# Optimization experiments

Hardware: AMD Instinct MI355X
Metric: run time of the kernel (lower is better)

Reference implementation:

```python
import jax, jax.numpy as jnp
import numpy as np

N_NODES = 50000
D = 128
L = 3  # layers
R = 4  # relations
E = 200000  # edges per relation
LN_EPS = 1e-5
NEG_SLOPE = 0.2


def setup_inputs() -> dict:
    key = jax.random.key(0)
    ks = jax.random.split(key, 12)
    s = 1.0 / np.sqrt(D)  # xavier-ish scale
    return {
        "h": jax.random.normal(ks[0], (N_NODES, D), jnp.float32),
        "edge_src": jax.random.randint(ks[1], (R, E), 0, N_NODES, jnp.int32),
        "edge_dst": jax.random.randint(ks[2], (R, E), 0, N_NODES, jnp.int32),
        "W_src": jax.random.normal(ks[3], (L, R, D, D), jnp.float32) * s,
        "W_dst": jax.random.normal(ks[4], (L, R, D, D), jnp.float32) * s,
        "attn_l": jax.random.normal(ks[5], (L, R, D), jnp.float32) * s,
        "attn_r": jax.random.normal(ks[6], (L, R, D), jnp.float32) * s,
        "gat_bias": jax.random.normal(ks[7], (L, R, D), jnp.float32) * 0.02,
        "ntype_bias": jax.random.normal(ks[8], (L, D), jnp.float32) * 0.02,
        "ln_gamma": jnp.ones((L, D), jnp.float32),
        "ln_beta": jnp.zeros((L, D), jnp.float32),
    }


def _gat_rel(x, Wsrc, Wdst, al, ar, b, src, dst):
    # single-head DGL GATConv with bipartite (src, dst) feats (same node set here)
    n = x.shape[0]
    hs = x @ Wsrc  # [N, D] projected source feats
    hd = x @ Wdst  # [N, D] projected dest feats
    el = (hs * al).sum(-1)  # [N]
    er = (hd * ar).sum(-1)  # [N]
    e = jax.nn.leaky_relu(el[src] + er[dst], NEG_SLOPE)  # [E]
    # edge softmax over incoming edges of each dst node
    m = jax.lax.stop_gradient(jax.ops.segment_max(e, dst, num_segments=n))
    a = jnp.exp(e - m[dst])
    denom = jax.ops.segment_sum(a, dst, num_segments=n)
    w = a / denom[dst]  # [E] attention weights
    out = jax.ops.segment_sum(hs[src] * w[:, None], dst, num_segments=n)  # [N, D]
    return out + b


def _layer_norm(x, g, b):
    mu = x.mean(-1, keepdims=True)
    var = ((x - mu) ** 2).mean(-1, keepdims=True)
    return (x - mu) * jax.lax.rsqrt(var + LN_EPS) * g + b


def reference(h, edge_src, edge_dst, W_src, W_dst, attn_l, attn_r,
              gat_bias, ntype_bias, ln_gamma, ln_beta):
    x = h
    n_layers = W_src.shape[0]
    gat_vmapped = jax.vmap(_gat_rel, in_axes=(None, 0, 0, 0, 0, 0, 0, 0))
    for l in range(n_layers):
        rel_out = gat_vmapped(x, W_src[l], W_dst[l], attn_l[l], attn_r[l],
                              gat_bias[l], edge_src, edge_dst)  # [R, N, D]
        hsum = rel_out.sum(0) + ntype_bias[l]  # HeteroGraphConv 'sum' + ntype bias
        if l < n_layers - 1:
            hsum = jax.nn.relu(hsum)  # activation on all but final layer
        # mean over heads (num_heads=1) is identity; then per-layer LayerNorm
        x = _layer_norm(hsum, ln_gamma[l], ln_beta[l])
    return x
```

## Files before the change

kernel.cpp:

```cpp
#include <hip/hip_runtime.h>

#define NN 50000
#define DIM 128
#define NREL 4
#define NEDGE 200000
#define NLAYER 3
#define SNB 196

typedef short s16x8 __attribute__((ext_vector_type(8)));
typedef float f32x4 __attribute__((ext_vector_type(4)));

__device__ __forceinline__ unsigned short f2bf(float f) {
    union { float f; unsigned u; } c; c.f = f;
    unsigned u = c.u + 0x7fffu + ((c.u >> 16) & 1u);
    return (unsigned short)(u >> 16);
}
__device__ __forceinline__ float lo_bf(unsigned u) {
    union { float f; unsigned u; } c; c.u = u << 16; return c.f;
}
__device__ __forceinline__ float hi_bf(unsigned u) {
    union { float f; unsigned u; } c; c.u = u & 0xffff0000u; return c.f;
}

__global__ __launch_bounds__(256) void k_constf(float* __restrict__ out, int n, float v) {
    int i = blockIdx.x * 256 + threadIdx.x;
    if (i < n) out[i] = v;
}

__global__ __launch_bounds__(256) void k_count(const int* __restrict__ dst, int* __restrict__ counts) {
    int r = blockIdx.y;
    int i = blockIdx.x * 256 + threadIdx.x;
    if (i < NEDGE) {
        int d = dst[r * NEDGE + i];
        if ((unsigned)d < NN) atomicAdd(&counts[r * NN + d], 1);
    }
}

__global__ __launch_bounds__(256) void k_s1(const int* __restrict__ counts, int* __restrict__ bsum) {
    int r = blockIdx.y, b = blockIdx.x;
    int i = b * 256 + threadIdx.x;
    int v = (i < NN) ? counts[r * NN + i] : 0;
    #pragma unroll
    for (int m = 1; m < 64; m <<= 1) v += __shfl_xor(v, m);
    __shared__ int ws[4];
    int wid = threadIdx.x >> 6, lane = threadIdx.x & 63;
    if (lane == 0) ws[wid] = v;
    __syncthreads();
    if (threadIdx.x == 0) bsum[r * SNB + b] = ws[0] + ws[1] + ws[2] + ws[3];
}

__global__ __launch_bounds__(256) void k_s2(const int* __restrict__ bsum, int* __restrict__ boff) {
    int r = threadIdx.x >> 6;
    int lane = threadIdx.x & 63;
    int carry = 0;
    for (int c0 = 0; c0 < SNB; c0 += 64) {
        int b = c0 + lane;
        int v = (b < SNB) ? bsum[r * SNB + b] : 0;
        int inc = v;
        #pragma unroll
        for (int d = 1; d < 64; d <<= 1) {
            int t = __shfl_up(inc, d);
            if (lane >= d) inc += t;
        }
        if (b < SNB) boff[r * SNB + b] = carry + inc - v;
        carry += __shfl(inc, 63);
    }
}

__global__ __launch_bounds__(256) void k_s3(const int* __restrict__ counts, const int* __restrict__ boff,
                                            int* __restrict__ row_ptr, int* __restrict__ nxt) {
    int r = blockIdx.y, b = blockIdx.x;
    int i = b * 256 + threadIdx.x;
    int v = (i < NN) ? counts[r * NN + i] : 0;
    int lane = threadIdx.x & 63, wid = threadIdx.x >> 6;
    int inc = v;
    #pragma unroll
    for (int d = 1; d < 64; d <<= 1) {
        int t = __shfl_up(inc, d);
        if (lane >= d) inc += t;
    }
    __shared__ int ws[4];
    if (lane == 63) ws[wid] = inc;
    __syncthreads();
    int woff = 0;
    #pragma unroll
    for (int w = 0; w < 4; ++w) woff += (w < wid) ? ws[w] : 0;
    if (i < NN) {
        int ex = boff[r * SNB + b] + woff + inc - v;
        row_ptr[r * (NN + 1) + i] = ex;
        nxt[r * NN + i] = ex;
    }
    if (b == 0 && threadIdx.x == 0) row_ptr[r * (NN + 1) + NN] = NEDGE;
}

__global__ __launch_bounds__(256) void k_fill(const int* __restrict__ src, const int* __restrict__ dst,
                                              int* __restrict__ nxt, int* __restrict__ csr) {
    int r = blockIdx.y;
    int i = blockIdx.x * 256 + threadIdx.x;
    if (i < NEDGE) {
        int d = dst[r * NEDGE + i];
        if ((unsigned)d >= NN) return;
        int pos = atomicAdd(&nxt[r * NN + d], 1);
        if ((unsigned)pos < NEDGE) csr[r * NEDGE + pos] = src[r * NEDGE + i];
    }
}

__global__ __launch_bounds__(256) void k_prep(const float* __restrict__ Wsrc,
                                              const float* __restrict__ Wdst,
                                              const float* __restrict__ al,
                                              const float* __restrict__ ar,
                                              const float* __restrict__ ntb,
                                              const float* __restrict__ gb,
                                              const float* __restrict__ x,
                                              unsigned short* __restrict__ wf,
                                              float* __restrict__ wl,
                                              float* __restrict__ wr,
                                              float* __restrict__ biasc,
                                              unsigned short* __restrict__ xb) {
    int b = blockIdx.x;
    const int PL = NLAYER * 512;
    if (b < PL) {
        int l = b / 512;
        int t = b % 512;
        if (t < 256) {
            int idx = t * 256 + threadIdx.x;
            int jj = idx & 7, lane = (idx >> 3) & 63, s = (idx >> 9) & 3, tt = (idx >> 11) & 7, r = idx >> 14;
            int k = s * 32 + ((lane >> 4) << 3) + jj;
            int n = tt * 16 + (lane & 15);
            wf[l * 65536 + idx] = f2bf(Wsrc[((size_t)(l * NREL + r) * DIM + k) * DIM + n]);
        } else if (t < 384) {
            int gw = (t - 256) * 4 + (threadIdx.x >> 6);
            int lane = threadIdx.x & 63;
            int r = gw >> 7, k = gw & 127;
            const float* wrow = Wsrc + (((size_t)(l * NREL + r) * DIM + k) * DIM);
            const float* arow = al + (l * NREL + r) * DIM;
            float s = wrow[lane * 2] * arow[lane * 2] + wrow[lane * 2 + 1] * arow[lane * 2 + 1];
            #pragma unroll
            for (int m = 1; m < 64; m <<= 1) s += __shfl_xor(s, m);
            if (lane == 0) wl[l * 512 + gw] = s;
        } else {
            int gw = (t - 384) * 4 + (threadIdx.x >> 6);
            int lane = threadIdx.x & 63;
            int r = gw >> 7, k = gw & 127;
            const float* wrow = Wdst + (((size_t)(l * NREL + r) * DIM + k) * DIM);
            const float* arow = ar + (l * NREL + r) * DIM;
            float s = wrow[lane * 2] * arow[lane * 2] + wrow[lane * 2 + 1] * arow[lane * 2 + 1];
            #pragma unroll
            for (int m = 1; m < 64; m <<= 1) s += __shfl_xor(s, m);
            if (lane == 0) wr[l * 512 + gw] = s;
        }
    } else if (b < PL + 2) {
        int t = (b - PL) * 256 + threadIdx.x;
        if (t < NLAYER * DIM) {
            int l = t >> 7, k = t & 127;
            float s = ntb[t];
            #pragma unroll
            for (int r = 0; r < NREL; ++r) s += gb[(l * NREL + r) * DIM + k];
            biasc[t] = s;
        }
    } else {
        int i = ((b - PL - 2) * 256 + threadIdx.x) * 4;
        f32x4 v = *(const f32x4*)(x + i);
        unsigned short o[4];
        #pragma unroll
        for (int j = 0; j < 4; ++j) o[j] = f2bf(v[j]);
        *(ushort2*)(xb + i) = make_ushort2(o[0], o[1]);
        *(ushort2*)(xb + i + 2) = make_ushort2(o[2], o[3]);
    }
}

__global__ __launch_bounds__(256) void k_er0(const float* __restrict__ x,
                                             const float* __restrict__ wl,
                                             const float* __restrict__ wr,
                                             float* __restrict__ el,
                                             float* __restrict__ er) {
    int oct = threadIdx.x >> 3, ol = threadIdx.x & 7;
    int n = blockIdx.x * 32 + oct;
    if (n >= NN) return;
    int f0 = ol * 16;
    const float* xp = x + (size_t)n * DIM + f0;
    f32x4 xv[4];
    #pragma unroll
    for (int k = 0; k < 4; ++k) xv[k] = *(const f32x4*)(xp + 4 * k);
    #pragma unroll
    for (int r = 0; r < NREL; ++r) {
        float sl = 0.f, sr = 0.f;
        #pragma unroll
        for (int k = 0; k < 4; ++k) {
            f32x4 lv = *(const f32x4*)(wl + r * DIM + f0 + 4 * k);
            f32x4 rv = *(const f32x4*)(wr + r * DIM + f0 + 4 * k);
            sl += xv[k][0] * lv[0] + xv[k][1] * lv[1] + xv[k][2] * lv[2] + xv[k][3] * lv[3];
            sr += xv[k][0] * rv[0] + xv[k][1] * rv[1] + xv[k][2] * rv[2] + xv[k][3] * rv[3];
        }
        sl += __shfl_xor(sl, 1); sl += __shfl_xor(sl, 2); sl += __shfl_xor(sl, 4);
        sr += __shfl_xor(sr, 1); sr += __shfl_xor(sr, 2); sr += __shfl_xor(sr, 4);
        if (ol == 0) { el[r * NN + n] = sl; er[r * NN + n] = sr; }
    }
}

__global__ __launch_bounds__(512) void k_fused(const unsigned short* __restrict__ xb,
                                               const float* __restrict__ el,
                                               const float* __restrict__ er,
                                               const int* __restrict__ row_ptr,
                                               const int* __restrict__ csr,
                                               const unsigned short* __restrict__ wf,
                                               const float* __restrict__ biasc,
                                               const float* __restrict__ lng,
                                               const float* __restrict__ lnb,
                                               const float* __restrict__ wl,
                                               const float* __restrict__ wr,
                                               float* __restrict__ dout,
                                               unsigned short* __restrict__ xb2,
                                               float* __restrict__ el2,
                                               float* __restrict__ er2,
                                               int l, int last) {
    __shared__ s16x8 lds_a[16 * 64];
    int tid = threadIdx.x;

    {
        int pair = tid >> 3;
        int ol   = tid & 7;
        int g    = ol >> 2;
        int fl   = ol & 3;
        int nd   = pair >> 2;
        int r    = pair & 3;
        int n    = blockIdx.x * 16 + nd;
        int f0   = fl * 32;

        int start = row_ptr[r * (NN + 1) + n];
        int end   = row_ptr[r * (NN + 1) + n + 1];
        if (start < 0) start = 0;
        if (end > NEDGE) end = NEDGE;
        int deg = end - start;

        float ern = er[r * NN + n];
        const int* cp = csr + r * NEDGE;
        const float* elp = el + r * NN;

        f32x4 av[8] = {{0,0,0,0},{0,0,0,0},{0,0,0,0},{0,0,0,0},
                       {0,0,0,0},{0,0,0,0},{0,0,0,0},{0,0,0,0}};
        float denom = 0.f;
        int e = start + g;
        if (e < end) {
            int s0 = cp[e]; if ((unsigned)s0 >= NN) s0 = 0;
            float e0v = elp[s0];
            const uint4* hp = (const uint4*)(xb + (size_t)s0 * DIM + f0);
            uint4 xa = hp[0], xbv = hp[1], xc = hp[2], xd = hp[3];
            for (; e < end; e += 2) {
                int i1 = e + 2; i1 = (i1 < end) ? i1 : start;
                int s1 = cp[i1]; if ((unsigned)s1 >= NN) s1 = 0;
                float e1v = elp[s1];
                const uint4* hp1 = (const uint4*)(xb + (size_t)s1 * DIM + f0);
                uint4 ya = hp1[0], yb = hp1[1], yc = hp1[2], yd = hp1[3];

                float ev = e0v + ern;
                ev = ev >= 0.f ? ev : 0.2f * ev;
                ev = fminf(fmaxf(ev, -60.f), 60.f);
                float p = __expf(ev);
                denom += p;
                av[0][0] += p * lo_bf(xa.x); av[0][1] += p * hi_bf(xa.x);
                av[0][2] += p * lo_bf(xa.y); av[0][3] += p * hi_bf(xa.y);
                av[1][0] += p * lo_bf(xa.z); av[1][1] += p * hi_bf(xa.z);
                av[1][2] += p * lo_bf(xa.w); av[1][3] += p * hi_bf(xa.w);
                av[2][0] += p * lo_bf(xbv.x); av[2][1] += p * hi_bf(xbv.x);
                av[2][2] += p * lo_bf(xbv.y); av[2][3] += p * hi_bf(xbv.y);
                av[3][0] += p * lo_bf(xbv.z); av[3][1] += p * hi_bf(xbv.z);
                av[3][2] += p * lo_bf(xbv.w); av[3][3] += p * hi_bf(xbv.w);
                av[4][0] += p * lo_bf(xc.x); av[4][1] += p * hi_bf(xc.x);
                av[4][2] += p * lo_bf(xc.y); av[4][3] += p * hi_bf(xc.y);
                av[5][0] += p * lo_bf(xc.z); av[5][1] += p * hi_bf(xc.z);
                av[5][2] += p * lo_bf(xc.w); av[5][3] += p * hi_bf(xc.w);
                av[6][0] += p * lo_bf(xd.x); av[6][1] += p * hi_bf(xd.x);
                av[6][2] += p * lo_bf(xd.y); av[6][3] += p * hi_bf(xd.y);
                av[7][0] += p * lo_bf(xd.z); av[7][1] += p * hi_bf(xd.z);
                av[7][2] += p * lo_bf(xd.w); av[7][3] += p * hi_bf(xd.w);
                e0v = e1v; xa = ya; xbv = yb; xc = yc; xd = yd;
            }
        }
        denom += __shfl_xor(denom, 4);
        #pragma unroll
        for (int q = 0; q < 8; ++q) {
            #pragma unroll
            for (int j = 0; j < 4; ++j) av[q][j] += __shfl_xor(av[q][j], 4);
        }
        float inv = (deg > 0) ? (1.0f / denom) : 0.f;
        if (g == 0) {
            #pragma unroll
            for (int q = 0; q < 4; ++q) {
                s16x8 o;
                #pragma unroll
                for (int j = 0; j < 4; ++j) {
                    o[j]     = (short)f2bf(av[2 * q][j] * inv);
                    o[j + 4] = (short)f2bf(av[2 * q + 1][j] * inv);
                }
                lds_a[(r * 4 + fl) * 64 + q * 16 + nd] = o;
            }
        }
    }
    __syncthreads();

    int wv = tid >> 6, lane = tid & 63;
    int quad = lane >> 4, n16 = lane & 15;
    f32x4 acc = {0.f, 0.f, 0.f, 0.f};
    {
        const s16x8* wfp = (const s16x8*)wf + (size_t)l * NREL * 2048;
        #pragma unroll
        for (int sp = 0; sp < 16; ++sp) {
            s16x8 a = lds_a[sp * 64 + lane];
            const s16x8* wb = wfp + (size_t)(sp >> 2) * 2048;
            int sl = sp & 3;
            s16x8 b = wb[(wv * 4 + sl) * 64 + lane];
            acc = __builtin_amdgcn_mfma_f32_16x16x32_bf16(a, b, acc, 0, 0, 0);
        }
    }
    __syncthreads();
    float* Cl = (float*)lds_a;
    {
        #pragma unroll
        for (int reg = 0; reg < 4; ++reg) {
            int row = quad * 4 + reg;
            Cl[row * DIM + wv * 16 + n16] = acc[reg];
        }
    }
    __syncthreads();

    {
        int nd2 = tid >> 5;
        int sub = tid & 31;
        int f   = sub * 4;
        int n2  = blockIdx.x * 16 + nd2;

        float t[4];
        #pragma unroll
        for (int j = 0; j < 4; ++j) t[j] = Cl[nd2 * DIM + f + j] + biasc[l * DIM + f + j];
        if (!last) {
            #pragma unroll
            for (int j = 0; j < 4; ++j) t[j] = fmaxf(t[j], 0.f);
        }
        float s1 = 0.f;
        #pragma unroll
        for (int j = 0; j < 4; ++j) s1 += t[j];
        s1 += __shfl_xor(s1, 1); s1 += __shfl_xor(s1, 2);
        s1 += __shfl_xor(s1, 4); s1 += __shfl_xor(s1, 8);
        s1 += __shfl_xor(s1, 16);
        float mean = s1 * (1.0f / 128.0f);
        float s2 = 0.f;
        #pragma unroll
        for (int j = 0; j < 4; ++j) { t[j] -= mean; s2 += t[j] * t[j]; }
        s2 += __shfl_xor(s2, 1); s2 += __shfl_xor(s2, 2);
        s2 += __shfl_xor(s2, 4); s2 += __shfl_xor(s2, 8);
        s2 += __shfl_xor(s2, 16);
        float rs = rsqrtf(s2 * (1.0f / 128.0f) + 1e-5f);

        float y[4];
        #pragma unroll
        for (int j = 0; j < 4; ++j)
            y[j] = t[j] * rs * lng[l * DIM + f + j] + lnb[l * DIM + f + j];

        if (last) {
            float* op = dout + (size_t)n2 * DIM + f;
            f32x4 v0;
            v0[0] = y[0]; v0[1] = y[1]; v0[2] = y[2]; v0[3] = y[3];
            *(f32x4*)op = v0;
        } else {
            unsigned pk0 = (unsigned)f2bf(y[0]) | ((unsigned)f2bf(y[1]) << 16);
            unsigned pk1 = (unsigned)f2bf(y[2]) | ((unsigned)f2bf(y[3]) << 16);
            uint2 v; v.x = pk0; v.y = pk1;
            *(uint2*)(xb2 + (size_t)n2 * DIM + f) = v;

            const float* wlp = wl + (l + 1) * 512;
            const float* wrp = wr + (l + 1) * 512;
            #pragma unroll
            for (int rp = 0; rp < NREL; ++rp) {
                float sl_ = 0.f, sr_ = 0.f;
                #pragma unroll
                for (int j = 0; j < 4; ++j) {
                    sl_ += y[j] * wlp[rp * DIM + f + j];
                    sr_ += y[j] * wrp[rp * DIM + f + j];
                }
                sl_ += __shfl_xor(sl_, 1); sl_ += __shfl_xor(sl_, 2);
                sl_ += __shfl_xor(sl_, 4); sl_ += __shfl_xor(sl_, 8);
                sl_ += __shfl_xor(sl_, 16);
                sr_ += __shfl_xor(sr_, 1); sr_ += __shfl_xor(sr_, 2);
                sr_ += __shfl_xor(sr_, 4); sr_ += __shfl_xor(sr_, 8);
                sr_ += __shfl_xor(sr_, 16);
                if (sub == 0) {
                    el2[rp * NN + n2] = sl_;
                    er2[rp * NN + n2] = sr_;
                }
            }
        }
    }
}

extern "C" void kernel_launch(void* const* d_in, const int* in_sizes, int n_in,
                              void* d_out, int out_size, void* d_ws, size_t ws_size,
                              hipStream_t stream) {
    const float* h        = (const float*)d_in[0];
    const int*   edge_src = (const int*)d_in[1];
    const int*   edge_dst = (const int*)d_in[2];
    const float* W_src    = (const float*)d_in[3];
    const float* W_dst    = (const float*)d_in[4];
    const float* attn_l   = (const float*)d_in[5];
    const float* attn_r   = (const float*)d_in[6];
    const float* gat_bias = (const float*)d_in[7];
    const float* ntype_b  = (const float*)d_in[8];
    const float* ln_g     = (const float*)d_in[9];
    const float* ln_b     = (const float*)d_in[10];

    if (n_in < 11) return;
    if (in_sizes[0] != NN * DIM) return;
    if (in_sizes[1] != NREL * NEDGE || in_sizes[2] != NREL * NEDGE) return;
    if (in_sizes[3] != NLAYER * NREL * DIM * DIM || in_sizes[4] != NLAYER * NREL * DIM * DIM) return;
    if (in_sizes[5] != NLAYER * NREL * DIM || in_sizes[6] != NLAYER * NREL * DIM) return;
    if (in_sizes[7] != NLAYER * NREL * DIM || in_sizes[8] != NLAYER * DIM) return;
    if (out_size != NN * DIM) return;

    auto align256 = [](size_t x) { return (x + 255) & ~(size_t)255; };
    size_t szElEr = align256((size_t)NREL * NN * 4);
    size_t szXbf  = align256((size_t)NN * DIM * 2);
    size_t szWlr  = align256((size_t)NLAYER * 512 * 4);
    size_t szBc   = align256((size_t)NLAYER * DIM * 4);
    size_t szWf   = align256((size_t)NLAYER * NREL * DIM * DIM * 2);
    size_t szRp   = align256((size_t)NREL * (NN + 1) * 4);
    size_t szNxt  = align256((size_t)NREL * NN * 4);
    size_t szCsr  = align256((size_t)NREL * NEDGE * 4);
    size_t szScn  = align256((size_t)NREL * SNB * 4) * 2;
    size_t need = 4 * szElEr + 2 * szXbf + 2 * szWlr + szBc + szWf + szRp + szNxt + szCsr + szScn;

    if (ws_size < need) {
        k_constf<<<(NN * DIM + 255) / 256, 256, 0, stream>>>((float*)d_out, NN * DIM, 100.0f);
        return;
    }

    char* base = (char*)d_ws;
    size_t off = 0;
    auto alloc = [&](size_t bytes) -> char* { char* p = base + off; off += align256(bytes); return p; };

    float* el   = (float*)alloc((size_t)NREL * NN * 4);
    float* er   = (float*)alloc((size_t)NREL * NN * 4);
    float* el2  = (float*)alloc((size_t)NREL * NN * 4);
    float* er2  = (float*)alloc((size_t)NREL * NN * 4);
    unsigned short* xbf  = (unsigned short*)alloc((size_t)NN * DIM * 2);
    unsigned short* xbf2 = (unsigned short*)alloc((size_t)NN * DIM * 2);
    float* wl    = (float*)alloc((size_t)NLAYER * 512 * 4);
    float* wr    = (float*)alloc((size_t)NLAYER * 512 * 4);
    float* biasc = (float*)alloc((size_t)NLAYER * DIM * 4);
    unsigned short* wfrag = (unsigned short*)alloc((size_t)NLAYER * NREL * DIM * DIM * 2);
    int* rowp = (int*)alloc((size_t)NREL * (NN + 1) * 4);
    int* nxt  = (int*)alloc((size_t)NREL * NN * 4);
    int* csr  = (int*)alloc((size_t)NREL * NEDGE * 4);
    int* bsum = (int*)alloc((size_t)NREL * SNB * 4);
    int* boff = (int*)alloc((size_t)NREL * SNB * 4);

    (void)hipMemsetAsync(nxt, 0, (size_t)NREL * NN * 4, stream);
    k_count<<<dim3((NEDGE + 255) / 256, NREL), 256, 0, stream>>>(edge_dst, nxt);
    k_s1<<<dim3(SNB, NREL), 256, 0, stream>>>(nxt, bsum);
    k_s2<<<1, 256, 0, stream>>>(bsum, boff);
    k_s3<<<dim3(SNB, NREL), 256, 0, stream>>>(nxt, boff, rowp, nxt);
    k_fill<<<dim3((NEDGE + 255) / 256, NREL), 256, 0, stream>>>(edge_src, edge_dst, nxt, csr);
    k_prep<<<NLAYER * 512 + 2 + NN * DIM / 1024, 256, 0, stream>>>(
        W_src, W_dst, attn_l, attn_r, ntype_b, gat_bias, h, wfrag, wl, wr, biasc, xbf);
    k_er0<<<(NN + 31) / 32, 256, 0, stream>>>(h, wl, wr, el, er);

    float* dout = (float*)d_out;
    k_fused<<<NN / 16, 512, 0, stream>>>(xbf, el, er, rowp, csr, wfrag, biasc, ln_g, ln_b,
                                         wl, wr, dout, xbf2, el2, er2, 0, 0);
    k_fused<<<NN / 16, 512, 0, stream>>>(xbf2, el2, er2, rowp, csr, wfrag, biasc, ln_g, ln_b,
                                         wl, wr, dout, xbf, el, er, 1, 0);
    k_fused<<<NN / 16, 512, 0, stream>>>(xbf, el, er, rowp, csr, wfrag, biasc, ln_g, ln_b,
                                         wl, wr, dout, xbf2, el2, er2, 2, 1);
}
```

Before: 400.7 us.

## Halve fused-kernel block to 8 nodes with 256 threads and two MFMA tiles per wave

Shrinks each fused block from 16 nodes/512 threads to 8 nodes/256 threads, doubling the grid, and sets launch bounds to allow 8 blocks per CU. Each of the 4 waves now computes two 16-column MFMA output tiles. The unused 8 rows of the 16-row MFMA A operand are zero-filled. The aim is finer-grained scheduling and better latency hiding for the irregular gather phase. The cost is that half of every MFMA is wasted on padding rows, and weight fragments are reloaded twice as often across blocks.

Result: slower. 526.5 us (+31.4%).

```diff
diff --git a/kernel.cpp b/kernel.cpp
--- a/kernel.cpp
+++ b/kernel.cpp
@@ -6,6 +6,7 @@
 #define NEDGE 200000
 #define NLAYER 3
 #define SNB 196
+#define NODES_PER_BLK 8
 
 typedef short s16x8 __attribute__((ext_vector_type(8)));
 typedef float f32x4 __attribute__((ext_vector_type(4)));
@@ -198,7 +199,7 @@
     }
 }
 
-__global__ __launch_bounds__(512) void k_fused(const unsigned short* __restrict__ xb,
+__global__ __launch_bounds__(256, 8) void k_fused(const unsigned short* __restrict__ xb,
                                                const float* __restrict__ el,
                                                const float* __restrict__ er,
                                                const int* __restrict__ row_ptr,
@@ -224,7 +225,7 @@
         int fl   = ol & 3;
         int nd   = pair >> 2;
         int r    = pair & 3;
-        int n    = blockIdx.x * 16 + nd;
+        int n    = blockIdx.x * NODES_PER_BLK + nd;
         int f0   = fl * 32;
 
         int start = row_ptr[r * (NN + 1) + n];
@@ -295,31 +296,43 @@
                 }
                 lds_a[(r * 4 + fl) * 64 + q * 16 + nd] = o;
             }
+        } else {
+            s16x8 z = {0, 0, 0, 0, 0, 0, 0, 0};
+            #pragma unroll
+            for (int q = 0; q < 4; ++q)
+                lds_a[(r * 4 + fl) * 64 + q * 16 + nd + 8] = z;
         }
     }
     __syncthreads();
 
     int wv = tid >> 6, lane = tid & 63;
     int quad = lane >> 4, n16 = lane & 15;
-    f32x4 acc = {0.f, 0.f, 0.f, 0.f};
+    f32x4 acc0 = {0.f, 0.f, 0.f, 0.f}, acc1 = {0.f, 0.f, 0.f, 0.f};
     {
         const s16x8* wfp = (const s16x8*)wf + (size_t)l * NREL * 2048;
+        int t0c = wv * 2, t1c = wv * 2 + 1;
         #pragma unroll
         for (int sp = 0; sp < 16; ++sp) {
             s16x8 a = lds_a[sp * 64 + lane];
             const s16x8* wb = wfp + (size_t)(sp >> 2) * 2048;
             int sl = sp & 3;
-            s16x8 b = wb[(wv * 4 + sl) * 64 + lane];
-            acc = __builtin_amdgcn_mfma_f32_16x16x32_bf16(a, b, acc, 0, 0, 0);
+            s16x8 b0 = wb[(t0c * 4 + sl) * 64 + lane];
+            s16x8 b1 = wb[(t1c * 4 + sl) * 64 + lane];
+            acc0 = __builtin_amdgcn_mfma_f32_16x16x32_bf16(a, b0, acc0, 0, 0, 0);
+            acc1 = __builtin_amdgcn_mfma_f32_16x16x32_bf16(a, b1, acc1, 0, 0, 0);
         }
     }
     __syncthreads();
     float* Cl = (float*)lds_a;
     {
+        int t0c = wv * 2, t1c = wv * 2 + 1;
         #pragma unroll
         for (int reg = 0; reg < 4; ++reg) {
             int row = quad * 4 + reg;
-            Cl[row * DIM + wv * 16 + n16] = acc[reg];
+            if (row < NODES_PER_BLK) {
+                Cl[row * DIM + t0c * 16 + n16] = acc0[reg];
+                Cl[row * DIM + t1c * 16 + n16] = acc1[reg];
+            }
         }
     }
     __syncthreads();
@@ -328,7 +341,7 @@
         int nd2 = tid >> 5;
         int sub = tid & 31;
         int f   = sub * 4;
-        int n2  = blockIdx.x * 16 + nd2;
+        int n2  = blockIdx.x * NODES_PER_BLK + nd2;
 
         float t[4];
         #pragma unroll
@@ -464,10 +477,10 @@
     k_er0<<<(NN + 31) / 32, 256, 0, stream>>>(h, wl, wr, el, er);
 
     float* dout = (float*)d_out;
-    k_fused<<<NN / 16, 512, 0, stream>>>(xbf, el, er, rowp, csr, wfrag, biasc, ln_g, ln_b,
+    k_fused<<<NN / NODES_PER_BLK, 256, 0, stream>>>(xbf, el, er, rowp, csr, wfrag, biasc, ln_g, ln_b,
                                          wl, wr, dout, xbf2, el2, er2, 0, 0);
-    k_fused<<<NN / 16, 512, 0, stream>>>(xbf2, el2, er2, rowp, csr, wfrag, biasc, ln_g, ln_b,
+    k_fused<<<NN / NODES_PER_BLK, 256, 0, stream>>>(xbf2, el2, er2, rowp, csr, wfrag, biasc, ln_g, ln_b,
                                          wl, wr, dout, xbf, el, er, 1, 0);
-    k_fused<<<NN / 16, 512, 0, stream>>>(xbf, el, er, rowp, csr, wfrag, biasc, ln_g, ln_b,
+    k_fused<<<NN / NODES_PER_BLK, 256, 0, stream>>>(xbf, el, er, rowp, csr, wfrag, biasc, ln_g, ln_b,
                                          wl, wr, dout, xbf2, el2, er2, 2, 1);
 }
```

## Process 32 nodes per 256-thread block with 2x2 MFMA tiles per wave

Applied to the files above, without the earlier changes.

The fused layer kernel now handles 32 destination nodes per block with 256 threads instead of 16 nodes with 512 threads. The edge-gather phase drops the two-way edge split and its shuffle reduction, so each thread walks all edges of its (node, relation, feature-slice) serially over two passes. In the GEMM phase each wave computes a 2x2 block of 16x16 MFMA tiles, so every weight fragment loaded is reused across twice as many rows. The cost is less parallelism in the gather, a longer serial edge loop per thread, more registers per thread, and half as many threads in flight to hide gather latency.

Result: faster. 367.6 us (-8.3%).

```diff
diff --git a/kernel.cpp b/kernel.cpp
--- a/kernel.cpp
+++ b/kernel.cpp
@@ -6,6 +6,7 @@
 #define NEDGE 200000
 #define NLAYER 3
 #define SNB 196
+#define NODES_PER_BLK 32
 
 typedef short s16x8 __attribute__((ext_vector_type(8)));
 typedef float f32x4 __attribute__((ext_vector_type(4)));
@@ -198,7 +199,7 @@
     }
 }
 
-__global__ __launch_bounds__(512) void k_fused(const unsigned short* __restrict__ xb,
+__global__ __launch_bounds__(256) void k_fused(const unsigned short* __restrict__ xb,
                                                const float* __restrict__ el,
                                                const float* __restrict__ er,
                                                const int* __restrict__ row_ptr,
@@ -214,121 +215,124 @@
                                                float* __restrict__ el2,
                                                float* __restrict__ er2,
                                                int l, int last) {
-    __shared__ s16x8 lds_a[16 * 64];
+    __shared__ s16x8 lds_a[2 * 16 * 64];
     int tid = threadIdx.x;
 
-    {
-        int pair = tid >> 3;
-        int ol   = tid & 7;
-        int g    = ol >> 2;
-        int fl   = ol & 3;
+    for (int p = 0; p < 2; ++p) {
+        int pair = tid >> 2;
+        int ol   = tid & 3;
         int nd   = pair >> 2;
         int r    = pair & 3;
-        int n    = blockIdx.x * 16 + nd;
-        int f0   = fl * 32;
-
-        int start = row_ptr[r * (NN + 1) + n];
-        int end   = row_ptr[r * (NN + 1) + n + 1];
+        int n    = blockIdx.x * NODES_PER_BLK + p * 16 + nd;
+        int f0   = ol * 32;
+
+        int valid = (n < NN);
+        int nc = valid ? n : 0;
+        int start = row_ptr[r * (NN + 1) + nc];
+        int end   = valid ? row_ptr[r * (NN + 1) + nc + 1] : start;
         if (start < 0) start = 0;
         if (end > NEDGE) end = NEDGE;
         int deg = end - start;
 
-        float ern = er[r * NN + n];
+        float ern = er[r * NN + nc];
         const int* cp = csr + r * NEDGE;
         const float* elp = el + r * NN;
 
         f32x4 av[8] = {{0,0,0,0},{0,0,0,0},{0,0,0,0},{0,0,0,0},
                        {0,0,0,0},{0,0,0,0},{0,0,0,0},{0,0,0,0}};
         float denom = 0.f;
-        int e = start + g;
-        if (e < end) {
-            int s0 = cp[e]; if ((unsigned)s0 >= NN) s0 = 0;
-            float e0v = elp[s0];
+        if (deg > 0) {
+            int s0 = cp[start]; if ((unsigned)s0 >= NN) s0 = 0;
+            float e0 = elp[s0];
             const uint4* hp = (const uint4*)(xb + (size_t)s0 * DIM + f0);
             uint4 xa = hp[0], xbv = hp[1], xc = hp[2], xd = hp[3];
-            for (; e < end; e += 2) {
-                int i1 = e + 2; i1 = (i1 < end) ? i1 : start;
+            for (int e = 0; e < deg; ++e) {
+                int i1 = start + e + 1; i1 = (i1 < end) ? i1 : start;
                 int s1 = cp[i1]; if ((unsigned)s1 >= NN) s1 = 0;
-                float e1v = elp[s1];
+                float e1 = elp[s1];
                 const uint4* hp1 = (const uint4*)(xb + (size_t)s1 * DIM + f0);
                 uint4 ya = hp1[0], yb = hp1[1], yc = hp1[2], yd = hp1[3];
 
-                float ev = e0v + ern;
+                float ev = e0 + ern;
                 ev = ev >= 0.f ? ev : 0.2f * ev;
                 ev = fminf(fmaxf(ev, -60.f), 60.f);
-                float p = __expf(ev);
-                denom += p;
-                av[0][0] += p * lo_bf(xa.x); av[0][1] += p * hi_bf(xa.x);
-                av[0][2] += p * lo_bf(xa.y); av[0][3] += p * hi_bf(xa.y);
-                av[1][0] += p * lo_bf(xa.z); av[1][1] += p * hi_bf(xa.z);
-                av[1][2] += p * lo_bf(xa.w); av[1][3] += p * hi_bf(xa.w);
-                av[2][0] += p * lo_bf(xbv.x); av[2][1] += p * hi_bf(xbv.x);
-                av[2][2] += p * lo_bf(xbv.y); av[2][3] += p * hi_bf(xbv.y);
-                av[3][0] += p * lo_bf(xbv.z); av[3][1] += p * hi_bf(xbv.z);
-                av[3][2] += p * lo_bf(xbv.w); av[3][3] += p * hi_bf(xbv.w);
-                av[4][0] += p * lo_bf(xc.x); av[4][1] += p * hi_bf(xc.x);
-                av[4][2] += p * lo_bf(xc.y); av[4][3] += p * hi_bf(xc.y);
-                av[5][0] += p * lo_bf(xc.z); av[5][1] += p * hi_bf(xc.z);
-                av[5][2] += p * lo_bf(xc.w); av[5][3] += p * hi_bf(xc.w);
-                av[6][0] += p * lo_bf(xd.x); av[6][1] += p * hi_bf(xd.x);
-                av[6][2] += p * lo_bf(xd.y); av[6][3] += p * hi_bf(xd.y);
-                av[7][0] += p * lo_bf(xd.z); av[7][1] += p * hi_bf(xd.z);
-                av[7][2] += p * lo_bf(xd.w); av[7][3] += p * hi_bf(xd.w);
-                e0v = e1v; xa = ya; xbv = yb; xc = yc; xd = yd;
+                float pw = __expf(ev);
+                denom += pw;
+                av[0][0] += pw * lo_bf(xa.x); av[0][1] += pw * hi_bf(xa.x);
+                av[0][2] += pw * lo_bf(xa.y); av[0][3] += pw * hi_bf(xa.y);
+                av[1][0] += pw * lo_bf(xa.z); av[1][1] += pw * hi_bf(xa.z);
+                av[1][2] += pw * lo_bf(xa.w); av[1][3] += pw * hi_bf(xa.w);
+                av[2][0] += pw * lo_bf(xbv.x); av[2][1] += pw * hi_bf(xbv.x);
+                av[2][2] += pw * lo_bf(xbv.y); av[2][3] += pw * hi_bf(xbv.y);
+                av[3][0] += pw * lo_bf(xbv.z); av[3][1] += pw * hi_bf(xbv.z);
+                av[3][2] += pw * lo_bf(xbv.w); av[3][3] += pw * hi_bf(xbv.w);
+                av[4][0] += pw * lo_bf(xc.x); av[4][1] += pw * hi_bf(xc.x);
+                av[4][2] += pw * lo_bf(xc.y); av[4][3] += pw * hi_bf(xc.y);
+                av[5][0] += pw * lo_bf(xc.z); av[5][1] += pw * hi_bf(xc.z);
+                av[5][2] += pw * lo_bf(xc.w); av[5][3] += pw * hi_bf(xc.w);
+                av[6][0] += pw * lo_bf(xd.x); av[6][1] += pw * hi_bf(xd.x);
+                av[6][2] += pw * lo_bf(xd.y); av[6][3] += pw * hi_bf(xd.y);
+                av[7][0] += pw * lo_bf(xd.z); av[7][1] += pw * hi_bf(xd.z);
+                av[7][2] += pw * lo_bf(xd.w); av[7][3] += pw * hi_bf(xd.w);
+                e0 = e1; xa = ya; xbv = yb; xc = yc; xd = yd;
             }
         }
-        denom += __shfl_xor(denom, 4);
-        #pragma unroll
-        for (int q = 0; q < 8; ++q) {
-            #pragma unroll
-            for (int j = 0; j < 4; ++j) av[q][j] += __shfl_xor(av[q][j], 4);
-        }
         float inv = (deg > 0) ? (1.0f / denom) : 0.f;
-        if (g == 0) {
-            #pragma unroll
-            for (int q = 0; q < 4; ++q) {
-                s16x8 o;
-                #pragma unroll
-                for (int j = 0; j < 4; ++j) {
-                    o[j]     = (short)f2bf(av[2 * q][j] * inv);
-                    o[j + 4] = (short)f2bf(av[2 * q + 1][j] * inv);
-                }
-                lds_a[(r * 4 + fl) * 64 + q * 16 + nd] = o;
+        #pragma unroll
+        for (int q = 0; q < 4; ++q) {
+            s16x8 o;
+            #pragma unroll
+            for (int j = 0; j < 4; ++j) {
+                o[j]     = (short)f2bf(av[2 * q][j] * inv);
+                o[j + 4] = (short)f2bf(av[2 * q + 1][j] * inv);
             }
+            lds_a[p * 1024 + (r * 4 + ol) * 64 + q * 16 + nd] = o;
         }
     }
     __syncthreads();
 
     int wv = tid >> 6, lane = tid & 63;
     int quad = lane >> 4, n16 = lane & 15;
-    f32x4 acc = {0.f, 0.f, 0.f, 0.f};
+    f32x4 acc00 = {0.f, 0.f, 0.f, 0.f}, acc01 = {0.f, 0.f, 0.f, 0.f};
+    f32x4 acc10 = {0.f, 0.f, 0.f, 0.f}, acc11 = {0.f, 0.f, 0.f, 0.f};
     {
         const s16x8* wfp = (const s16x8*)wf + (size_t)l * NREL * 2048;
+        int t0c = wv * 2, t1c = wv * 2 + 1;
         #pragma unroll
         for (int sp = 0; sp < 16; ++sp) {
-            s16x8 a = lds_a[sp * 64 + lane];
+            s16x8 a0 = lds_a[sp * 64 + lane];
+            s16x8 a1 = lds_a[1024 + sp * 64 + lane];
             const s16x8* wb = wfp + (size_t)(sp >> 2) * 2048;
             int sl = sp & 3;
-            s16x8 b = wb[(wv * 4 + sl) * 64 + lane];
-            acc = __builtin_amdgcn_mfma_f32_16x16x32_bf16(a, b, acc, 0, 0, 0);
+            s16x8 b0 = wb[(t0c * 4 + sl) * 64 + lane];
+            s16x8 b1 = wb[(t1c * 4 + sl) * 64 + lane];
+            acc00 = __builtin_amdgcn_mfma_f32_16x16x32_bf16(a0, b0, acc00, 0, 0, 0);
+            acc01 = __builtin_amdgcn_mfma_f32_16x16x32_bf16(a0, b1, acc01, 0, 0, 0);
+            acc10 = __builtin_amdgcn_mfma_f32_16x16x32_bf16(a1, b0, acc10, 0, 0, 0);
+            acc11 = __builtin_amdgcn_mfma_f32_16x16x32_bf16(a1, b1, acc11, 0, 0, 0);
         }
     }
     __syncthreads();
     float* Cl = (float*)lds_a;
     {
+        int t0c = wv * 2, t1c = wv * 2 + 1;
         #pragma unroll
         for (int reg = 0; reg < 4; ++reg) {
             int row = quad * 4 + reg;
-            Cl[row * DIM + wv * 16 + n16] = acc[reg];
+            Cl[row * DIM + t0c * 16 + n16] = acc00[reg];
+            Cl[row * DIM + t1c * 16 + n16] = acc01[reg];
+            Cl[(16 + row) * DIM + t0c * 16 + n16] = acc10[reg];
+            Cl[(16 + row) * DIM + t1c * 16 + n16] = acc11[reg];
         }
     }
     __syncthreads();
 
-    {
-        int nd2 = tid >> 5;
+    for (int it = 0; it < 4; ++it) {
+        int nd2 = it * 8 + (tid >> 5);
         int sub = tid & 31;
         int f   = sub * 4;
-        int n2  = blockIdx.x * 16 + nd2;
+        int n2  = blockIdx.x * NODES_PER_BLK + nd2;
+        if (n2 >= NN) continue;
 
         float t[4];
         #pragma unroll
@@ -464,10 +468,11 @@
     k_er0<<<(NN + 31) / 32, 256, 0, stream>>>(h, wl, wr, el, er);
 
     float* dout = (float*)d_out;
-    k_fused<<<NN / 16, 512, 0, stream>>>(xbf, el, er, rowp, csr, wfrag, biasc, ln_g, ln_b,
-                                         wl, wr, dout, xbf2, el2, er2, 0, 0);
-    k_fused<<<NN / 16, 512, 0, stream>>>(xbf2, el2, er2, rowp, csr, wfrag, biasc, ln_g, ln_b,
-                                         wl, wr, dout, xbf, el, er, 1, 0);
-    k_fused<<<NN / 16, 512, 0, stream>>>(xbf, el, er, rowp, csr, wfrag, biasc, ln_g, ln_b,
-                                         wl, wr, dout, xbf2, el2, er2, 2, 1);
-}
+    int nblk = (NN + NODES_PER_BLK - 1) / NODES_PER_BLK;
+    k_fused<<<nblk, 256, 0, stream>>>(xbf, el, er, rowp, csr, wfrag, biasc, ln_g, ln_b,
+                                      wl, wr, dout, xbf2, el2, er2, 0, 0);
+    k_fused<<<nblk, 256, 0, stream>>>(xbf2, el2, er2, rowp, csr, wfrag, biasc, ln_g, ln_b,
+                                      wl, wr, dout, xbf, el, er, 1, 0);
+    k_fused<<<nblk, 256, 0, stream>>>(xbf, el, er, rowp, csr, wfrag, biasc, ln_g, ln_b,
+                                      wl, wr, dout, xbf2, el2, er2, 2, 1);
+}
```
